# Optimization experiments

Measured on AMD Instinct MI355X. Metric: run time of the kernel, lower is better.

Reference implementation:

```python
import jax, jax.numpy as jnp
import numpy as np

B = 16384      # batch of (user, item) interactions
N = 819200     # total packed implicit-history items (~50 per user)
U = 100000     # num_users
I = 100000     # num_items
D = 64         # emb_dim


def setup_inputs() -> dict:
    key = jax.random.key(0)
    ks = jax.random.split(key, 8)
    user_ids = jax.random.randint(ks[0], (B,), 0, U)
    item_ids = jax.random.randint(ks[1], (B,), 0, I)
    offsets = jnp.sort(jax.random.randint(ks[2], (B,), 0, N)).at[0].set(0)
    flat_implicit = jax.random.randint(ks[3], (N,), 0, I)
    user_emb = 0.1 * jax.random.normal(ks[4], (U, D), dtype=jnp.float32)
    item_emb = 0.1 * jax.random.normal(ks[5], (I, D), dtype=jnp.float32)
    implicit_item_emb = 0.1 * jax.random.normal(ks[6], (I, D), dtype=jnp.float32)
    user_bias = jnp.zeros((U, 1), dtype=jnp.float32)
    item_bias = jnp.zeros((I, 1), dtype=jnp.float32)
    global_bias = jnp.zeros((1,), dtype=jnp.float32)
    return {"user_ids": user_ids, "item_ids": item_ids, "offsets": offsets,
            "flat_implicit": flat_implicit, "user_emb": user_emb,
            "item_emb": item_emb, "implicit_item_emb": implicit_item_emb,
            "user_bias": user_bias, "item_bias": item_bias,
            "global_bias": global_bias}


def reference(user_ids, item_ids, offsets, flat_implicit, user_emb, item_emb,
              implicit_item_emb, user_bias, item_bias, global_bias):
    n = flat_implicit.shape[0]
    b = offsets.shape[0]
    u = user_emb[user_ids]                       # [B, D]
    i = item_emb[item_ids]                       # [B, D]
    imp = implicit_item_emb[flat_implicit]       # [N, D]
    # ragged segment ids from start offsets (empty segments get no rows)
    seg_ids = jnp.searchsorted(offsets, jnp.arange(n), side="right") - 1
    summed = jax.ops.segment_sum(imp, seg_ids, num_segments=b)  # [B, D]
    sizes = jnp.diff(jnp.concatenate([offsets, jnp.array([n], dtype=offsets.dtype)]))
    norm = jnp.where(sizes > 0, jnp.sqrt(sizes.astype(jnp.float32)), 1.0)
    final_user = u + summed / norm[:, None]
    dot = jnp.sum(final_user * i, axis=1)        # [B]
    pred = dot + user_bias[user_ids][:, 0] + item_bias[item_ids][:, 0] + global_bias
    return pred
```

## Files before the change

### kernel.cpp

```cpp
#include <hip/hip_runtime.h>
#include <math.h>


#define K1_WAVES 4

__global__ void svdpp_zero(float* __restrict__ out, int B)
{
    const int i = blockIdx.x * blockDim.x + threadIdx.x;
    if (i < B) out[i] = 0.f;
}

#define LOADIDX(d) const int idx##d = __shfl(my_idx, (sub << 4) | (d), 64);
#define LOADVAL(d) const float4 v##d = impv[(size_t)idx##d * 16 + l16];

#define FLUSH()                                                              \
    {                                                                        \
        float p = acc.x * i4.x + acc.y * i4.y + acc.z * i4.z + acc.w * i4.w; \
        p += __shfl_xor(p, 1, 64);                                           \
        p += __shfl_xor(p, 2, 64);                                           \
        p += __shfl_xor(p, 4, 64);                                           \
        p += __shfl_xor(p, 8, 64);                                           \
        if (l16 == 0) atomicAdd(&out[cur], p);                               \
    }

#define STEP(d)                                                              \
    {                                                                        \
        const int sd = __shfl(seg, (sub << 4) | (d), 64);                    \
        if (sd != cur) {                                                     \
            FLUSH();                                                         \
            cur = sd;                                                        \
            i4  = ((const float4*)(item_emb + (size_t)item_ids[cur] * 64))[l16]; \
            acc = make_float4(0.f, 0.f, 0.f, 0.f);                           \
        }                                                                    \
        if (base + (sub << 4) + (d) < N) {                                   \
            acc.x += v##d.x; acc.y += v##d.y;                                \
            acc.z += v##d.z; acc.w += v##d.w;                                \
        }                                                                    \
    }

__global__ __launch_bounds__(256, 1) void svdpp_gather(
    const int* __restrict__ item_ids,
    const int* __restrict__ offsets,
    const int* __restrict__ flat_implicit,
    const float* __restrict__ item_emb,
    const float* __restrict__ imp_emb,
    float* __restrict__ out,
    int B, int N)
{
    const int wave = threadIdx.x >> 6;
    const int lane = threadIdx.x & 63;
    const int base = (blockIdx.x * K1_WAVES + wave) << 6;
    if (base >= N) return;

    const int sub = lane >> 4;
    const int l16 = lane & 15;

    const int a  = base + lane;
    const int ac = (a < N) ? a : (N - 1);

    const int my_idx = flat_implicit[ac];

    int lo = 0, hi = B;
    while (lo < hi) {
        const int mid = (lo + hi) >> 1;
        if (offsets[mid] <= ac) lo = mid + 1; else hi = mid;
    }
    const int seg = lo - 1;

    int cur = __shfl(seg, sub << 4, 64);
    float4 i4 = ((const float4*)(item_emb + (size_t)item_ids[cur] * 64))[l16];
    float4 acc = make_float4(0.f, 0.f, 0.f, 0.f);

    const float4* impv = (const float4*)imp_emb;
    LOADIDX(0)  LOADIDX(1)  LOADIDX(2)  LOADIDX(3)
    LOADIDX(4)  LOADIDX(5)  LOADIDX(6)  LOADIDX(7)
    LOADIDX(8)  LOADIDX(9)  LOADIDX(10) LOADIDX(11)
    LOADIDX(12) LOADIDX(13) LOADIDX(14) LOADIDX(15)

    LOADVAL(0)  LOADVAL(1)  LOADVAL(2)  LOADVAL(3)
    LOADVAL(4)  LOADVAL(5)  LOADVAL(6)  LOADVAL(7)
    LOADVAL(8)  LOADVAL(9)  LOADVAL(10) LOADVAL(11)
    LOADVAL(12) LOADVAL(13) LOADVAL(14) LOADVAL(15)

    __builtin_amdgcn_sched_barrier(0);

    STEP(0)  STEP(1)  STEP(2)  STEP(3)
    STEP(4)  STEP(5)  STEP(6)  STEP(7)
    STEP(8)  STEP(9)  STEP(10) STEP(11)
    STEP(12) STEP(13) STEP(14) STEP(15)

    FLUSH();
}

__global__ __launch_bounds__(256, 1) void svdpp_final(
    const int* __restrict__ user_ids,
    const int* __restrict__ item_ids,
    const int* __restrict__ offsets,
    const float* __restrict__ user_emb,
    const float* __restrict__ item_emb,
    const float* __restrict__ user_bias,
    const float* __restrict__ item_bias,
    const float* __restrict__ global_bias,
    float* __restrict__ out,
    int B, int N)
{
    const int l16 = threadIdx.x & 15;
    const int b   = blockIdx.x * 16 + (threadIdx.x >> 4);
    if (b >= B) return;

    const int user = user_ids[b];
    const int item = item_ids[b];

    const float4 u4 = ((const float4*)(user_emb + (size_t)user * 64))[l16];
    const float4 i4 = ((const float4*)(item_emb + (size_t)item * 64))[l16];

    float p = u4.x * i4.x + u4.y * i4.y + u4.z * i4.z + u4.w * i4.w;
    p += __shfl_xor(p, 1, 64);
    p += __shfl_xor(p, 2, 64);
    p += __shfl_xor(p, 4, 64);
    p += __shfl_xor(p, 8, 64);

    if (l16 == 0) {
        const int start = offsets[b];
        const int end   = (b + 1 < B) ? offsets[b + 1] : N;
        const int n     = end - start;
        const float norm = (n > 0) ? sqrtf((float)n) : 1.f;
        out[b] = p + out[b] / norm + user_bias[item == item ? user : user]
               + item_bias[item] + global_bias[0];
    }
}

extern "C" void kernel_launch(void* const* d_in, const int* in_sizes, int n_in,
                              void* d_out, int out_size, void* d_ws, size_t ws_size,
                              hipStream_t stream) {
    const int*   user_ids      = (const int*)  d_in[0];
    const int*   item_ids      = (const int*)  d_in[1];
    const int*   offsets       = (const int*)  d_in[2];
    const int*   flat_implicit = (const int*)  d_in[3];
    const float* user_emb      = (const float*)d_in[4];
    const float* item_emb      = (const float*)d_in[5];
    const float* imp_emb       = (const float*)d_in[6];
    const float* user_bias     = (const float*)d_in[7];
    const float* item_bias     = (const float*)d_in[8];
    const float* global_bias   = (const float*)d_in[9];
    float* out = (float*)d_out;

    const int B = in_sizes[0];
    const int N = in_sizes[3];

    svdpp_zero<<<(B + 255) / 256, 256, 0, stream>>>(out, B);

    const int waves = (N + 63) / 64;
    const int g1 = (waves + K1_WAVES - 1) / K1_WAVES;
    svdpp_gather<<<g1, K1_WAVES * 64, 0, stream>>>(
        item_ids, offsets, flat_implicit, item_emb, imp_emb, out, B, N);

    svdpp_final<<<(B + 15) / 16, 256, 0, stream>>>(
        user_ids, item_ids, offsets, user_emb, item_emb,
        user_bias, item_bias, global_bias, out, B, N);
}
```

Measured before the change: 152.9 us.

## Partition gather by item-id residue across 8 block groups for cache locality

```diff
diff --git a/kernel.cpp b/kernel.cpp
--- a/kernel.cpp
+++ b/kernel.cpp
@@ -2,16 +2,21 @@
 #include <math.h>
 
 
-#define K1_WAVES 4
+typedef float f4 __attribute__((ext_vector_type(4)));
 
-__global__ void svdpp_zero(float* __restrict__ out, int B)
-{
-    const int i = blockIdx.x * blockDim.x + threadIdx.x;
-    if (i < B) out[i] = 0.f;
+#define CHUNK  512
+#define SUPERS 8
+#define QCAP   512
+#define WPB    4
+
+template <typename T>
+__device__ __forceinline__ T ntload(const T* p) {
+    return __builtin_nontemporal_load(const_cast<T*>(p));
 }
 
-#define LOADIDX(d) const int idx##d = __shfl(my_idx, (sub << 4) | (d), 64);
-#define LOADVAL(d) const float4 v##d = impv[(size_t)idx##d * 16 + l16];
+
+#define GIDX(d) const int pk##d = __shfl(pk, 16 * sub + (d), 64);
+#define GVAL(d) const f4 v##d = impv[(size_t)(pk##d & 0x1FFFF) * 16 + l16];
 
 #define FLUSH()                                                              \
     {                                                                        \
@@ -20,21 +25,24 @@
         p += __shfl_xor(p, 2, 64);                                           \
         p += __shfl_xor(p, 4, 64);                                           \
         p += __shfl_xor(p, 8, 64);                                           \
-        if (l16 == 0) atomicAdd(&out[cur], p);                               \
+        const int s0 = offsets[cur];                                         \
+        const int e0 = (cur + 1 < B) ? offsets[cur + 1] : N;                 \
+        const float invn = 1.0f / sqrtf((float)(e0 - s0));                   \
+        if (l16 == 0) atomicAdd(&out[cur], p * invn);                        \
     }
 
-#define STEP(d)                                                              \
+#define ASTEP(d)                                                             \
     {                                                                        \
-        const int sd = __shfl(seg, (sub << 4) | (d), 64);                    \
-        if (sd != cur) {                                                     \
-            FLUSH();                                                         \
-            cur = sd;                                                        \
-            i4  = ((const float4*)(item_emb + (size_t)item_ids[cur] * 64))[l16]; \
-            acc = make_float4(0.f, 0.f, 0.f, 0.f);                           \
-        }                                                                    \
-        if (base + (sub << 4) + (d) < N) {                                   \
-            acc.x += v##d.x; acc.y += v##d.y;                                \
-            acc.z += v##d.z; acc.w += v##d.w;                                \
+        const int e = tb + 16 * sub + (d);                                   \
+        if (e < qcount) {                                                    \
+            const int sd = pk##d >> 17;                                      \
+            if (sd != cur) {                                                 \
+                FLUSH();                                                     \
+                cur = sd;                                                    \
+                i4  = ntload(&item4[(size_t)item_ids[cur] * 16 + l16]);      \
+                acc = (f4)(0.f);                                             \
+            }                                                                \
+            acc += v##d;                                                     \
         }                                                                    \
     }
 
@@ -47,49 +55,78 @@
     float* __restrict__ out,
     int B, int N)
 {
+    __shared__ int lq[WPB][QCAP];
+
+    const int k    = blockIdx.x & 7;
     const int wave = threadIdx.x >> 6;
     const int lane = threadIdx.x & 63;
-    const int base = (blockIdx.x * K1_WAVES + wave) << 6;
+    const int base = ((blockIdx.x >> 3) * WPB + wave) * CHUNK;
     if (base >= N) return;
 
     const int sub = lane >> 4;
     const int l16 = lane & 15;
 
-    const int a  = base + lane;
-    const int ac = (a < N) ? a : (N - 1);
+    int* const myq = lq[wave];
+    int qcount = 0;
 
-    const int my_idx = flat_implicit[ac];
+    #pragma unroll
+    for (int s = 0; s < SUPERS; ++s) {
+        const int pos = base + s * 64 + lane;
+        int  idx  = 0;
+        int  seg  = 0;
+        bool qok  = false;
+        if (pos < N) {
+            idx = ntload(&flat_implicit[pos]);
+            qok = ((idx & 7) == k);
+            if (qok) {
+                int lo = 0, hi = B;
+                while (lo < hi) {
+                    const int mid = (lo + hi) >> 1;
+                    if (offsets[mid] <= pos) lo = mid + 1; else hi = mid;
+                }
+                seg = lo - 1;
+            }
+        }
+        const unsigned long long m = __ballot(qok);
+        const int rank = __popcll(m & ((1ull << lane) - 1ull));
+        if (qok) myq[qcount + rank] = (seg << 17) | idx;
+        qcount += __popcll(m);
+    }
 
-    int lo = 0, hi = B;
-    while (lo < hi) {
-        const int mid = (lo + hi) >> 1;
-        if (offsets[mid] <= ac) lo = mid + 1; else hi = mid;
+    asm volatile("s_waitcnt lgkmcnt(0)" ::: "memory");
+
+    const f4* impv  = (const f4*)imp_emb;
+    const f4* item4 = (const f4*)item_emb;
+
+    for (int tb = 0; tb < qcount; tb += 64) {
+        const int ec = min(tb + lane, qcount - 1);
+        const int pk = myq[ec];
+
+        GIDX(0)  GIDX(1)  GIDX(2)  GIDX(3)
+        GIDX(4)  GIDX(5)  GIDX(6)  GIDX(7)
+        GIDX(8)  GIDX(9)  GIDX(10) GIDX(11)
+        GIDX(12) GIDX(13) GIDX(14) GIDX(15)
+
+        GVAL(0)  GVAL(1)  GVAL(2)  GVAL(3)
+        GVAL(4)  GVAL(5)  GVAL(6)  GVAL(7)
+        GVAL(8)  GVAL(9)  GVAL(10) GVAL(11)
+        GVAL(12) GVAL(13) GVAL(14) GVAL(15)
+
+        __builtin_amdgcn_sched_barrier(0);
+
+        const bool hasAny = (tb + 16 * sub) < qcount;
+        int cur = pk0 >> 17;
+        f4  acc = (f4)(0.f);
+        f4  i4  = (f4)(0.f);
+        if (hasAny) i4 = ntload(&item4[(size_t)item_ids[cur] * 16 + l16]);
+
+        ASTEP(0)  ASTEP(1)  ASTEP(2)  ASTEP(3)
+        ASTEP(4)  ASTEP(5)  ASTEP(6)  ASTEP(7)
+        ASTEP(8)  ASTEP(9)  ASTEP(10) ASTEP(11)
+        ASTEP(12) ASTEP(13) ASTEP(14) ASTEP(15)
+
+        if (hasAny) FLUSH();
     }
-    const int seg = lo - 1;
-
-    int cur = __shfl(seg, sub << 4, 64);
-    float4 i4 = ((const float4*)(item_emb + (size_t)item_ids[cur] * 64))[l16];
-    float4 acc = make_float4(0.f, 0.f, 0.f, 0.f);
-
-    const float4* impv = (const float4*)imp_emb;
-    LOADIDX(0)  LOADIDX(1)  LOADIDX(2)  LOADIDX(3)
-    LOADIDX(4)  LOADIDX(5)  LOADIDX(6)  LOADIDX(7)
-    LOADIDX(8)  LOADIDX(9)  LOADIDX(10) LOADIDX(11)
-    LOADIDX(12) LOADIDX(13) LOADIDX(14) LOADIDX(15)
-
-    LOADVAL(0)  LOADVAL(1)  LOADVAL(2)  LOADVAL(3)
-    LOADVAL(4)  LOADVAL(5)  LOADVAL(6)  LOADVAL(7)
-    LOADVAL(8)  LOADVAL(9)  LOADVAL(10) LOADVAL(11)
-    LOADVAL(12) LOADVAL(13) LOADVAL(14) LOADVAL(15)
-
-    __builtin_amdgcn_sched_barrier(0);
-
-    STEP(0)  STEP(1)  STEP(2)  STEP(3)
-    STEP(4)  STEP(5)  STEP(6)  STEP(7)
-    STEP(8)  STEP(9)  STEP(10) STEP(11)
-    STEP(12) STEP(13) STEP(14) STEP(15)
-
-    FLUSH();
 }
 
 __global__ __launch_bounds__(256, 1) void svdpp_final(
@@ -111,8 +148,8 @@
     const int user = user_ids[b];
     const int item = item_ids[b];
 
-    const float4 u4 = ((const float4*)(user_emb + (size_t)user * 64))[l16];
-    const float4 i4 = ((const float4*)(item_emb + (size_t)item * 64))[l16];
+    const f4 u4 = ((const f4*)user_emb)[(size_t)user * 16 + l16];
+    const f4 i4 = ((const f4*)item_emb)[(size_t)item * 16 + l16];
 
     float p = u4.x * i4.x + u4.y * i4.y + u4.z * i4.z + u4.w * i4.w;
     p += __shfl_xor(p, 1, 64);
@@ -121,12 +158,7 @@
     p += __shfl_xor(p, 8, 64);
 
     if (l16 == 0) {
-        const int start = offsets[b];
-        const int end   = (b + 1 < B) ? offsets[b + 1] : N;
-        const int n     = end - start;
-        const float norm = (n > 0) ? sqrtf((float)n) : 1.f;
-        out[b] = p + out[b] / norm + user_bias[item == item ? user : user]
-               + item_bias[item] + global_bias[0];
+        out[b] += p + user_bias[user] + item_bias[item] + global_bias[0];
     }
 }
 
@@ -148,11 +180,11 @@
     const int B = in_sizes[0];
     const int N = in_sizes[3];
 
-    svdpp_zero<<<(B + 255) / 256, 256, 0, stream>>>(out, B);
+    hipMemsetAsync(out, 0, (size_t)B * sizeof(float), stream);
 
-    const int waves = (N + 63) / 64;
-    const int g1 = (waves + K1_WAVES - 1) / K1_WAVES;
-    svdpp_gather<<<g1, K1_WAVES * 64, 0, stream>>>(
+    const int nchunks = (N + CHUNK - 1) / CHUNK;
+    const int blocks  = 8 * ((nchunks + WPB - 1) / WPB);
+    svdpp_gather<<<blocks, WPB * 64, 0, stream>>>(
         item_ids, offsets, flat_implicit, item_emb, imp_emb, out, B, N);
 
     svdpp_final<<<(B + 15) / 16, 256, 0, stream>>>(
```

Result: slower. 283.3 us (+85.3%).
